# Kernel optimization log

Hardware: AMD Instinct MI355X
Metric: run time of the kernel (lower is better)

The kernel has to match this reference:

```python
import jax, jax.numpy as jnp
import numpy as np

B, T, E, H = 4, 1024, 1024, 16
D = E // H  # head_dim = 64


def setup_inputs() -> dict:
    key = jax.random.key(0)
    ks = jax.random.split(key, 6)
    s = 0.02  # realistic init scale for stable softmax
    return {
        "hidden_states": jax.random.normal(ks[0], (B, T, E), jnp.float32),
        "attention_mask": jnp.zeros((B, 1, T, T), jnp.float32),
        "Wq": jax.random.normal(ks[1], (E, E), jnp.float32) * s,
        "bq": jnp.zeros((E,), jnp.float32),
        "Wk": jax.random.normal(ks[2], (E, E), jnp.float32) * s,
        "bk": jnp.zeros((E,), jnp.float32),
        "Wv": jax.random.normal(ks[3], (E, E), jnp.float32) * s,
        "bv": jnp.zeros((E,), jnp.float32),
        "Wo": jax.random.normal(ks[4], (E, E), jnp.float32) * s,
        "bo": jnp.zeros((E,), jnp.float32),
    }


def reference(hidden_states, attention_mask, Wq, bq, Wk, bk, Wv, bv, Wo, bo):
    b, t, e = hidden_states.shape
    scaling = jnp.asarray(D, hidden_states.dtype) ** -0.5
    # q_proj weights/bias are pre-scaled in the module; equivalent to scaling q output
    q = (hidden_states @ Wq.T + bq) * scaling      # [B,T,E]
    k = hidden_states @ Wk.T + bk                   # self-attention path (no cache)
    v = hidden_states @ Wv.T + bv
    q = q.reshape(b, t, H, D)
    k = k.reshape(b, t, H, D)
    v = v.reshape(b, t, H, D)
    # bmm(q, k^T): [B,H,T,S] score matrix (materialized, as in the original)
    scores = jnp.einsum("bthd,bshd->bhts", q, k) + attention_mask
    probs = jax.nn.softmax(scores, axis=-1)
    ctx = jnp.einsum("bhts,bshd->bthd", probs, v).reshape(b, t, e)
    return ctx @ Wo.T + bo
```

## Files before the change

### kernel.cpp

```cpp
#include <hip/hip_runtime.h>
#include <math.h>

#define BB 4
#define TT 1024
#define EE 1024
#define HH 16
#define DD 64
#define KDIM 1024
#define N_HS (4096 * 1024)
#define N_W  (1024 * 1024)
#define NQKV (BB * HH * TT * DD)

typedef _Float16 f16x8 __attribute__((ext_vector_type(8)));
typedef float    f32x4 __attribute__((ext_vector_type(4)));

__device__ __forceinline__ unsigned short f2h(float x) {
    _Float16 h = (_Float16)x;
    return __builtin_bit_cast(unsigned short, h);
}
__device__ __forceinline__ void split_h(float x, unsigned short& hi, unsigned short& lo) {
    _Float16 h = (_Float16)x;
    hi = __builtin_bit_cast(unsigned short, h);
    lo = f2h(x - (float)h);
}

__device__ __forceinline__ void gload16(const void* g, void* l) {
    __builtin_amdgcn_global_load_lds(
        (const __attribute__((address_space(1))) void*)g,
        (__attribute__((address_space(3))) void*)l, 16, 0, 0);
}

__global__ __launch_bounds__(256)
void split_kernel(const float* __restrict__ hs,
                  const float* __restrict__ Wq, const float* __restrict__ Wk,
                  const float* __restrict__ Wv, const float* __restrict__ Wo,
                  unsigned short* __restrict__ ws)
{
    const int u = blockIdx.x * 256 + threadIdx.x;
    const float* src;
    unsigned short* dst;
    if (u < (N_HS / 4)) {
        src = hs + (size_t)u * 4;
        dst = ws + (size_t)u * 4;
    } else {
        int v = u - N_HS / 4;
        int wsel = v >> 18;
        int wo   = v & 0x3FFFF;
        const float* Wsrc = (wsel == 0) ? Wq : (wsel == 1) ? Wk : (wsel == 2) ? Wv : Wo;
        src = Wsrc + (size_t)wo * 4;
        dst = ws + (size_t)N_HS + (size_t)wsel * N_W + (size_t)wo * 4;
    }
    float4 x = *(const float4*)src;
    ushort4 h4;
    h4.x = f2h(x.x); h4.y = f2h(x.y); h4.z = f2h(x.z); h4.w = f2h(x.w);
    *(ushort4*)dst = h4;
}

__global__ __launch_bounds__(256)
void qkv_kernel(const unsigned short* __restrict__ hsp,
                const unsigned short* __restrict__ wqp,
                const float* __restrict__ bq, const float* __restrict__ bk,
                const float* __restrict__ bv,
                unsigned short* __restrict__ qkvb)
{
    __shared__ unsigned short Ah[128 * 32], Bh[128 * 32];

    const int widx  = blockIdx.x >> 3;
    const int nbase = (blockIdx.x & 7) * 128;
    const int mbase = blockIdx.y * 128;
    const unsigned short* Wp = wqp + (size_t)widx * N_W;
    const float* bias = (widx == 0) ? bq : (widx == 1) ? bk : bv;
    unsigned short* dst = qkvb + (size_t)widx * NQKV;
    const float scale = (widx == 0) ? 0.125f : 1.0f;

    const int tid  = threadIdx.x;
    const int w    = tid >> 6;
    const int lane = tid & 63;
    const int quad = lane >> 4;
    const int l16  = lane & 15;
    const int wm   = (w >> 1) * 64;
    const int wn   = (w & 1) * 64;

    f32x4 acc[4][4];
#pragma unroll
    for (int i = 0; i < 4; i++)
#pragma unroll
        for (int j = 0; j < 4; j++) acc[i][j] = (f32x4)0.f;

#pragma unroll 1
    for (int kt = 0; kt < KDIM; kt += 32) {
        __syncthreads();
#pragma unroll
        for (int i = 0; i < 2; i++) {
            int u = tid + i * 256;
            int r = u >> 2, c = u & 3;
            int q = c ^ ((r >> 1) & 3);
            gload16(hsp + (size_t)(mbase + r) * KDIM + kt + q * 8, &Ah[u * 8]);
            gload16(Wp  + (size_t)(nbase + r) * KDIM + kt + q * 8, &Bh[u * 8]);
        }
        __syncthreads();

        f16x8 af[4], bfr[4];
#pragma unroll
        for (int i = 0; i < 4; i++) {
            int r = wm + i * 16 + l16;
            af[i] = *(const f16x8*)&Ah[(r * 4 + (quad ^ ((r >> 1) & 3))) * 8];
        }
#pragma unroll
        for (int j = 0; j < 4; j++) {
            int r = wn + j * 16 + l16;
            bfr[j] = *(const f16x8*)&Bh[(r * 4 + (quad ^ ((r >> 1) & 3))) * 8];
        }
#pragma unroll
        for (int i = 0; i < 4; i++)
#pragma unroll
            for (int j = 0; j < 4; j++)
                acc[i][j] = __builtin_amdgcn_mfma_f32_16x16x32_f16(af[i], bfr[j], acc[i][j], 0, 0, 0);
    }

#pragma unroll
    for (int j = 0; j < 4; j++) {
        int n = nbase + wn + j * 16 + l16;
        int h = n >> 6, d = n & 63;
        float bj = bias[n];
#pragma unroll
        for (int i = 0; i < 4; i++)
#pragma unroll
            for (int rr = 0; rr < 4; rr++) {
                int m = mbase + wm + i * 16 + quad * 4 + rr;
                int b = m >> 10, t = m & 1023;
                dst[(((size_t)(b * HH + h) * TT + t) * DD + d)] =
                    f2h((acc[i][j][rr] + bj) * scale);
            }
    }
}

__global__ __launch_bounds__(256)
void vtrans_kernel(const unsigned short* __restrict__ vp,
                   unsigned short* __restrict__ vtp)
{
    __shared__ unsigned short Ts[64 * 72];
    const int bh = blockIdx.y;
    const int t0 = blockIdx.x * 64;
    const unsigned short* src = vp  + (size_t)bh * TT * DD + (size_t)t0 * DD;
    unsigned short*       dst = vtp + (size_t)bh * DD * TT + t0;
    const int tid = threadIdx.x;

#pragma unroll
    for (int i = 0; i < 2; i++) {
        int id = tid + i * 256;
        int r = id >> 3, c = id & 7;
        *(uint4*)&Ts[r * 72 + c * 8] = *(const uint4*)(src + (size_t)r * DD + c * 8);
    }
    __syncthreads();
#pragma unroll
    for (int i = 0; i < 2; i++) {
        int id = tid + i * 256;
        int d = id >> 3, c = id & 7;
        unsigned short tmp[8];
#pragma unroll
        for (int j = 0; j < 8; j++) tmp[j] = Ts[(c * 8 + j) * 72 + d];
        uint4 o;
        o.x = (unsigned int)tmp[0] | ((unsigned int)tmp[1] << 16);
        o.y = (unsigned int)tmp[2] | ((unsigned int)tmp[3] << 16);
        o.z = (unsigned int)tmp[4] | ((unsigned int)tmp[5] << 16);
        o.w = (unsigned int)tmp[6] | ((unsigned int)tmp[7] << 16);
        *(uint4*)(dst + (size_t)d * TT + c * 8) = o;
    }
}

__global__ __launch_bounds__(256)
void outproj_kernel(const unsigned short* __restrict__ ctxh,
                    const unsigned short* __restrict__ ctxl,
                    const unsigned short* __restrict__ wop,
                    const float* __restrict__ bo, float* __restrict__ out)
{
    __shared__ unsigned short Ach[64 * 32], Acl[64 * 32], Bh[128 * 32];

    const int nbase = blockIdx.x * 128;
    const int mbase = blockIdx.y * 64;

    const int tid  = threadIdx.x;
    const int w    = tid >> 6;
    const int lane = tid & 63;
    const int quad = lane >> 4;
    const int l16  = lane & 15;
    const int wm   = (w >> 1) * 32;
    const int wn   = (w & 1) * 64;

    f32x4 acc[2][4];
#pragma unroll
    for (int i = 0; i < 2; i++)
#pragma unroll
        for (int j = 0; j < 4; j++) acc[i][j] = (f32x4)0.f;

#pragma unroll 1
    for (int kt = 0; kt < KDIM; kt += 32) {
        __syncthreads();
        {
            int r = tid >> 2, c = tid & 3;
            int q = c ^ ((r >> 1) & 3);
            size_t ga = (size_t)(mbase + r) * KDIM + kt + q * 8;
            gload16(ctxh + ga, &Ach[tid * 8]);
            gload16(ctxl + ga, &Acl[tid * 8]);
        }
#pragma unroll
        for (int i = 0; i < 2; i++) {
            int u = tid + i * 256;
            int r = u >> 2, c = u & 3;
            int q = c ^ ((r >> 1) & 3);
            gload16(wop + (size_t)(nbase + r) * KDIM + kt + q * 8, &Bh[u * 8]);
        }
        __syncthreads();

        f16x8 ah[2], al[2], bfr[4];
#pragma unroll
        for (int i = 0; i < 2; i++) {
            int r = wm + i * 16 + l16;
            int slot = (r * 4 + (quad ^ ((r >> 1) & 3))) * 8;
            ah[i] = *(const f16x8*)&Ach[slot];
            al[i] = *(const f16x8*)&Acl[slot];
        }
#pragma unroll
        for (int j = 0; j < 4; j++) {
            int r = wn + j * 16 + l16;
            bfr[j] = *(const f16x8*)&Bh[(r * 4 + (quad ^ ((r >> 1) & 3))) * 8];
        }
#pragma unroll
        for (int i = 0; i < 2; i++)
#pragma unroll
            for (int j = 0; j < 4; j++) {
                acc[i][j] = __builtin_amdgcn_mfma_f32_16x16x32_f16(ah[i], bfr[j], acc[i][j], 0, 0, 0);
                acc[i][j] = __builtin_amdgcn_mfma_f32_16x16x32_f16(al[i], bfr[j], acc[i][j], 0, 0, 0);
            }
    }

#pragma unroll
    for (int j = 0; j < 4; j++) {
        int n = nbase + wn + j * 16 + l16;
        float bj = bo[n];
#pragma unroll
        for (int i = 0; i < 2; i++)
#pragma unroll
            for (int rr = 0; rr < 4; rr++) {
                int m = mbase + wm + i * 16 + quad * 4 + rr;
                out[(size_t)m * EE + n] = acc[i][j][rr] + bj;
            }
    }
}

#define LS 72

__global__ __launch_bounds__(256)
void attn_kernel(const unsigned short* __restrict__ qp_, const unsigned short* __restrict__ kp_,
                 const unsigned short* __restrict__ vtp_,
                 const float* __restrict__ mask,
                 unsigned short* __restrict__ ctxh, unsigned short* __restrict__ ctxl)
{
    __shared__ unsigned short Ks[64 * 64];
    __shared__ unsigned short Vt[64 * 64];
    __shared__ unsigned short Ps[64 * LS];

    const int bh = blockIdx.y;
    const int b  = bh >> 4;
    const int h  = bh & 15;
    const int m0 = blockIdx.x * 64;
    const size_t hoff = (size_t)bh * TT * DD;
    const unsigned short* qhp = qp_ + hoff;
    const unsigned short* khp = kp_ + hoff;
    const unsigned short* vtp = vtp_ + hoff;
    const float* mb = mask + (size_t)b * TT * TT;

    const int tid  = threadIdx.x;
    const int w    = tid >> 6;
    const int lane = tid & 63;
    const int quad = lane >> 4;
    const int l16  = lane & 15;

    f16x8 qf[2];
#pragma unroll
    for (int s = 0; s < 2; s++)
        qf[s] = *(const f16x8*)(qhp + (size_t)(m0 + w * 16 + l16) * DD + s * 32 + quad * 8);

    f32x4 o[4];
    float m_i[4], l_i[4];
#pragma unroll
    for (int t = 0; t < 4; t++) o[t] = (f32x4)0.f;
#pragma unroll
    for (int r = 0; r < 4; r++) { m_i[r] = -INFINITY; l_i[r] = 0.f; }

    for (int n0 = 0; n0 < TT; n0 += 64) {
        f32x4 st[4];
#pragma unroll
        for (int t = 0; t < 4; t++)
#pragma unroll
            for (int r = 0; r < 4; r++)
                st[t][r] = mb[(size_t)(m0 + w * 16 + quad * 4 + r) * TT + n0 + 16 * t + l16];

        __syncthreads();
#pragma unroll
        for (int i = 0; i < 2; i++) {
            int u = tid + i * 256;
            int r = u >> 3, cp = u & 7;
            int c = cp ^ (r & 7);
            gload16(khp + (size_t)(n0 + r) * DD + c * 8, &Ks[u * 8]);
            gload16(vtp + (size_t)r * TT + n0 + c * 8,   &Vt[u * 8]);
        }
        __syncthreads();

#pragma unroll
        for (int s = 0; s < 2; s++)
#pragma unroll
            for (int t = 0; t < 4; t++) {
                int R = 16 * t + l16;
                const f16x8 kf = *(const f16x8*)&Ks[(R * 8 + ((s * 4 + quad) ^ (R & 7))) * 8];
                st[t] = __builtin_amdgcn_mfma_f32_16x16x32_f16(qf[s], kf, st[t], 0, 0, 0);
            }

        float rm[4], rs[4], alpha[4];
#pragma unroll
        for (int r = 0; r < 4; r++)
            rm[r] = fmaxf(fmaxf(st[0][r], st[1][r]), fmaxf(st[2][r], st[3][r]));
#pragma unroll
        for (int mky = 1; mky < 16; mky <<= 1)
#pragma unroll
            for (int r = 0; r < 4; r++)
                rm[r] = fmaxf(rm[r], __shfl_xor(rm[r], mky));
#pragma unroll
        for (int r = 0; r < 4; r++) {
            float mn = fmaxf(m_i[r], rm[r]);
            alpha[r] = __expf(m_i[r] - mn);
            m_i[r]   = mn;
            rs[r]    = 0.f;
        }
#pragma unroll
        for (int t = 0; t < 4; t++)
#pragma unroll
            for (int r = 0; r < 4; r++) {
                float p = __expf(st[t][r] - m_i[r]);
                st[t][r] = p;
                rs[r] += p;
            }
#pragma unroll
        for (int mky = 1; mky < 16; mky <<= 1)
#pragma unroll
            for (int r = 0; r < 4; r++)
                rs[r] += __shfl_xor(rs[r], mky);
#pragma unroll
        for (int r = 0; r < 4; r++)
            l_i[r] = l_i[r] * alpha[r] + rs[r];
#pragma unroll
        for (int t = 0; t < 4; t++)
#pragma unroll
            for (int r = 0; r < 4; r++)
                o[t][r] *= alpha[r];

#pragma unroll
        for (int t = 0; t < 4; t++)
#pragma unroll
            for (int r = 0; r < 4; r++)
                Ps[(w * 16 + quad * 4 + r) * LS + 16 * t + l16] = f2h(st[t][r]);

#pragma unroll
        for (int s = 0; s < 2; s++) {
            const f16x8 pf = *(const f16x8*)&Ps[(w * 16 + l16) * LS + s * 32 + quad * 8];
#pragma unroll
            for (int t = 0; t < 4; t++) {
                int R = 16 * t + l16;
                const f16x8 vf = *(const f16x8*)&Vt[(R * 8 + ((s * 4 + quad) ^ (R & 7))) * 8];
                o[t] = __builtin_amdgcn_mfma_f32_16x16x32_f16(pf, vf, o[t], 0, 0, 0);
            }
        }
    }

#pragma unroll
    for (int r = 0; r < 4; r++) {
        float inv = 1.0f / l_i[r];
        int m = m0 + w * 16 + quad * 4 + r;
#pragma unroll
        for (int t = 0; t < 4; t++) {
            float val = o[t][r] * inv;
            unsigned short hi, lo;
            split_h(val, hi, lo);
            size_t off = (size_t)(b * TT + m) * EE + h * DD + 16 * t + l16;
            ctxh[off] = hi;
            ctxl[off] = lo;
        }
    }
}

extern "C" void kernel_launch(void* const* d_in, const int* in_sizes, int n_in,
                              void* d_out, int out_size, void* d_ws, size_t ws_size,
                              hipStream_t stream)
{
    const float* hs   = (const float*)d_in[0];
    const float* mask = (const float*)d_in[1];
    const float* Wq   = (const float*)d_in[2];
    const float* bq   = (const float*)d_in[3];
    const float* Wk   = (const float*)d_in[4];
    const float* bk   = (const float*)d_in[5];
    const float* Wv   = (const float*)d_in[6];
    const float* bv   = (const float*)d_in[7];
    const float* Wo   = (const float*)d_in[8];
    const float* bo   = (const float*)d_in[9];
    float* out = (float*)d_out;

    unsigned short* ws   = (unsigned short*)d_ws;
    unsigned short* hsp  = ws;
    unsigned short* wqp  = ws + (size_t)N_HS;
    unsigned short* wop  = wqp + 3 * (size_t)N_W;
    unsigned short* qkvb = wqp + 4 * (size_t)N_W;
    unsigned short* qp   = qkvb;
    unsigned short* kp   = qp + (size_t)NQKV;
    unsigned short* vp   = kp + (size_t)NQKV;
    unsigned short* ctxh = ws;
    unsigned short* ctxl = qkvb + 3 * (size_t)NQKV;
    unsigned short* vtp  = ctxl + (size_t)N_HS;

    split_kernel<<<8192, 256, 0, stream>>>(hs, Wq, Wk, Wv, Wo, ws);
    qkv_kernel<<<dim3(24, 32), 256, 0, stream>>>(hsp, wqp, bq, bk, bv, qkvb);
    vtrans_kernel<<<dim3(TT / 64, BB * HH), 256, 0, stream>>>(vp, vtp);
    attn_kernel<<<dim3(TT / 64, BB * HH), 256, 0, stream>>>(qp, kp, vtp, mask, ctxh, ctxl);
    outproj_kernel<<<dim3(8, 64), 256, 0, stream>>>(ctxh, ctxl, wop, bo, out);
}
```

Before: 232.4 us.

## Restructure attention as transposed S^T with double-buffered K/V and exp2 softmax

The attention kernel now computes transposed scores (K·Q^T) so each lane owns one query row, which removes most cross-lane shuffles. Probabilities stay in registers and feed a 16x16x16 MFMA directly instead of round-tripping through an LDS P tile. K/V tiles are double-buffered so the next tile loads while the current one computes, and exp2 with log2e folded into the Q scale and mask replaces exp. To make this work, a new kernel transposes and prescales the mask into workspace, which adds an extra 16 MB read and write pass and needs more workspace.

```diff
diff --git a/kernel.cpp b/kernel.cpp
--- a/kernel.cpp
+++ b/kernel.cpp
@@ -10,8 +10,10 @@
 #define N_HS (4096 * 1024)
 #define N_W  (1024 * 1024)
 #define NQKV (BB * HH * TT * DD)
+#define LOG2E 1.44269504088896340736f
 
 typedef _Float16 f16x8 __attribute__((ext_vector_type(8)));
+typedef _Float16 f16x4 __attribute__((ext_vector_type(4)));
 typedef float    f32x4 __attribute__((ext_vector_type(4)));
 
 __device__ __forceinline__ unsigned short f2h(float x) {
@@ -57,6 +59,38 @@
 }
 
 __global__ __launch_bounds__(256)
+void mtrans_kernel(const float* __restrict__ mask, float* __restrict__ mt)
+{
+    __shared__ float Ts[64][65];
+    const int b  = blockIdx.y;
+    const int m0 = (blockIdx.x & 15) * 64;
+    const int n0 = (blockIdx.x >> 4) * 64;
+    const float* src = mask + ((size_t)b * TT + m0) * TT + n0;
+    float*       dst = mt   + ((size_t)b * TT + n0) * TT + m0;
+    const int tid = threadIdx.x;
+#pragma unroll
+    for (int i = 0; i < 4; i++) {
+        int id = tid + i * 256;
+        int r = id >> 4, c = id & 15;
+        float4 v = *(const float4*)(src + (size_t)r * TT + c * 4);
+        Ts[r][c * 4 + 0] = v.x; Ts[r][c * 4 + 1] = v.y;
+        Ts[r][c * 4 + 2] = v.z; Ts[r][c * 4 + 3] = v.w;
+    }
+    __syncthreads();
+#pragma unroll
+    for (int i = 0; i < 4; i++) {
+        int id = tid + i * 256;
+        int d = id >> 4, c = id & 15;
+        float4 o;
+        o.x = Ts[c * 4 + 0][d] * LOG2E;
+        o.y = Ts[c * 4 + 1][d] * LOG2E;
+        o.z = Ts[c * 4 + 2][d] * LOG2E;
+        o.w = Ts[c * 4 + 3][d] * LOG2E;
+        *(float4*)(dst + (size_t)d * TT + c * 4) = o;
+    }
+}
+
+__global__ __launch_bounds__(256)
 void qkv_kernel(const unsigned short* __restrict__ hsp,
                 const unsigned short* __restrict__ wqp,
                 const float* __restrict__ bq, const float* __restrict__ bk,
@@ -71,7 +105,7 @@
     const unsigned short* Wp = wqp + (size_t)widx * N_W;
     const float* bias = (widx == 0) ? bq : (widx == 1) ? bk : bv;
     unsigned short* dst = qkvb + (size_t)widx * NQKV;
-    const float scale = (widx == 0) ? 0.125f : 1.0f;
+    const float scale = (widx == 0) ? 0.125f * LOG2E : 1.0f;
 
     const int tid  = threadIdx.x;
     const int w    = tid >> 6;
@@ -249,17 +283,14 @@
     }
 }
 
-#define LS 72
-
 __global__ __launch_bounds__(256)
 void attn_kernel(const unsigned short* __restrict__ qp_, const unsigned short* __restrict__ kp_,
                  const unsigned short* __restrict__ vtp_,
-                 const float* __restrict__ mask,
+                 const float* __restrict__ mtp,
                  unsigned short* __restrict__ ctxh, unsigned short* __restrict__ ctxl)
 {
-    __shared__ unsigned short Ks[64 * 64];
-    __shared__ unsigned short Vt[64 * 64];
-    __shared__ unsigned short Ps[64 * LS];
+    __shared__ unsigned short Ks[2][64 * 64];
+    __shared__ unsigned short Vt[2][64 * 64];
 
     const int bh = blockIdx.y;
     const int b  = bh >> 4;
@@ -269,124 +300,133 @@
     const unsigned short* qhp = qp_ + hoff;
     const unsigned short* khp = kp_ + hoff;
     const unsigned short* vtp = vtp_ + hoff;
-    const float* mb = mask + (size_t)b * TT * TT;
+    const float* mb = mtp + (size_t)b * TT * TT;
 
     const int tid  = threadIdx.x;
     const int w    = tid >> 6;
     const int lane = tid & 63;
     const int quad = lane >> 4;
     const int l16  = lane & 15;
+    const int m    = m0 + w * 16 + l16;
 
     f16x8 qf[2];
 #pragma unroll
     for (int s = 0; s < 2; s++)
-        qf[s] = *(const f16x8*)(qhp + (size_t)(m0 + w * 16 + l16) * DD + s * 32 + quad * 8);
-
-    f32x4 o[4];
-    float m_i[4], l_i[4];
-#pragma unroll
-    for (int t = 0; t < 4; t++) o[t] = (f32x4)0.f;
-#pragma unroll
-    for (int r = 0; r < 4; r++) { m_i[r] = -INFINITY; l_i[r] = 0.f; }
-
-    for (int n0 = 0; n0 < TT; n0 += 64) {
+        qf[s] = *(const f16x8*)(qhp + (size_t)m * DD + s * 32 + quad * 8);
+
+    f32x4 o2[4];
+#pragma unroll
+    for (int u = 0; u < 4; u++) o2[u] = (f32x4)0.f;
+    float m_i = -INFINITY, l_i = 0.f;
+
+#pragma unroll
+    for (int i = 0; i < 2; i++) {
+        int u = tid + i * 256;
+        int r = u >> 3, cp = u & 7;
+        int c = cp ^ (r & 7);
+        gload16(khp + (size_t)r * DD + c * 8, &Ks[0][u * 8]);
+        gload16(vtp + (size_t)r * TT + c * 8, &Vt[0][u * 8]);
+    }
+    __syncthreads();
+
+#pragma unroll 2
+    for (int it = 0; it < 16; ++it) {
+        const int n0  = it * 64;
+        const int cur = it & 1;
+
         f32x4 st[4];
 #pragma unroll
         for (int t = 0; t < 4; t++)
 #pragma unroll
             for (int r = 0; r < 4; r++)
-                st[t][r] = mb[(size_t)(m0 + w * 16 + quad * 4 + r) * TT + n0 + 16 * t + l16];
-
-        __syncthreads();
-#pragma unroll
-        for (int i = 0; i < 2; i++) {
-            int u = tid + i * 256;
-            int r = u >> 3, cp = u & 7;
-            int c = cp ^ (r & 7);
-            gload16(khp + (size_t)(n0 + r) * DD + c * 8, &Ks[u * 8]);
-            gload16(vtp + (size_t)r * TT + n0 + c * 8,   &Vt[u * 8]);
-        }
-        __syncthreads();
-
+                st[t][r] = mb[(size_t)(n0 + 16 * t + quad * 4 + r) * TT + m];
+
+        if (it < 15) {
+#pragma unroll
+            for (int i = 0; i < 2; i++) {
+                int u = tid + i * 256;
+                int r = u >> 3, cp = u & 7;
+                int c = cp ^ (r & 7);
+                gload16(khp + (size_t)(n0 + 64 + r) * DD + c * 8, &Ks[cur ^ 1][u * 8]);
+                gload16(vtp + (size_t)r * TT + n0 + 64 + c * 8,   &Vt[cur ^ 1][u * 8]);
+            }
+        }
+
+        __builtin_amdgcn_s_setprio(1);
 #pragma unroll
         for (int s = 0; s < 2; s++)
 #pragma unroll
             for (int t = 0; t < 4; t++) {
                 int R = 16 * t + l16;
-                const f16x8 kf = *(const f16x8*)&Ks[(R * 8 + ((s * 4 + quad) ^ (R & 7))) * 8];
-                st[t] = __builtin_amdgcn_mfma_f32_16x16x32_f16(qf[s], kf, st[t], 0, 0, 0);
-            }
-
-        float rm[4], rs[4], alpha[4];
-#pragma unroll
-        for (int r = 0; r < 4; r++)
-            rm[r] = fmaxf(fmaxf(st[0][r], st[1][r]), fmaxf(st[2][r], st[3][r]));
-#pragma unroll
-        for (int mky = 1; mky < 16; mky <<= 1)
-#pragma unroll
-            for (int r = 0; r < 4; r++)
-                rm[r] = fmaxf(rm[r], __shfl_xor(rm[r], mky));
-#pragma unroll
-        for (int r = 0; r < 4; r++) {
-            float mn = fmaxf(m_i[r], rm[r]);
-            alpha[r] = __expf(m_i[r] - mn);
-            m_i[r]   = mn;
-            rs[r]    = 0.f;
-        }
+                const f16x8 kf = *(const f16x8*)&Ks[cur][(R * 8 + ((s * 4 + quad) ^ (R & 7))) * 8];
+                st[t] = __builtin_amdgcn_mfma_f32_16x16x32_f16(kf, qf[s], st[t], 0, 0, 0);
+            }
+        __builtin_amdgcn_s_setprio(0);
+
+        float rm0 = fmaxf(fmaxf(st[0][0], st[0][1]), fmaxf(st[0][2], st[0][3]));
+        float rm1 = fmaxf(fmaxf(st[1][0], st[1][1]), fmaxf(st[1][2], st[1][3]));
+        float rm2 = fmaxf(fmaxf(st[2][0], st[2][1]), fmaxf(st[2][2], st[2][3]));
+        float rm3 = fmaxf(fmaxf(st[3][0], st[3][1]), fmaxf(st[3][2], st[3][3]));
+        float rm  = fmaxf(fmaxf(rm0, rm1), fmaxf(rm2, rm3));
+        rm = fmaxf(rm, __shfl_xor(rm, 16));
+        rm = fmaxf(rm, __shfl_xor(rm, 32));
+        float mn    = fmaxf(m_i, rm);
+        float alpha = exp2f(m_i - mn);
+        m_i = mn;
+        float rs = 0.f;
 #pragma unroll
         for (int t = 0; t < 4; t++)
 #pragma unroll
             for (int r = 0; r < 4; r++) {
-                float p = __expf(st[t][r] - m_i[r]);
+                float p = exp2f(st[t][r] - mn);
                 st[t][r] = p;
-                rs[r] += p;
-            }
-#pragma unroll
-        for (int mky = 1; mky < 16; mky <<= 1)
-#pragma unroll
-            for (int r = 0; r < 4; r++)
-                rs[r] += __shfl_xor(rs[r], mky);
-#pragma unroll
-        for (int r = 0; r < 4; r++)
-            l_i[r] = l_i[r] * alpha[r] + rs[r];
-#pragma unroll
-        for (int t = 0; t < 4; t++)
-#pragma unroll
-            for (int r = 0; r < 4; r++)
-                o[t][r] *= alpha[r];
-
-#pragma unroll
-        for (int t = 0; t < 4; t++)
-#pragma unroll
-            for (int r = 0; r < 4; r++)
-                Ps[(w * 16 + quad * 4 + r) * LS + 16 * t + l16] = f2h(st[t][r]);
-
-#pragma unroll
-        for (int s = 0; s < 2; s++) {
-            const f16x8 pf = *(const f16x8*)&Ps[(w * 16 + l16) * LS + s * 32 + quad * 8];
+                rs += p;
+            }
+        rs += __shfl_xor(rs, 16);
+        rs += __shfl_xor(rs, 32);
+        l_i = l_i * alpha + rs;
+
+        f16x4 pb[4];
+#pragma unroll
+        for (int t = 0; t < 4; t++) {
+            f16x4 pv;
+            pv[0] = (_Float16)st[t][0]; pv[1] = (_Float16)st[t][1];
+            pv[2] = (_Float16)st[t][2]; pv[3] = (_Float16)st[t][3];
+            pb[t] = pv;
+        }
+
+#pragma unroll
+        for (int u = 0; u < 4; u++)
+#pragma unroll
+            for (int rr = 0; rr < 4; rr++) o2[u][rr] *= alpha;
+
+        __builtin_amdgcn_s_setprio(1);
+#pragma unroll
+        for (int u = 0; u < 4; u++) {
+            int R = 16 * u + l16;
 #pragma unroll
             for (int t = 0; t < 4; t++) {
-                int R = 16 * t + l16;
-                const f16x8 vf = *(const f16x8*)&Vt[(R * 8 + ((s * 4 + quad) ^ (R & 7))) * 8];
-                o[t] = __builtin_amdgcn_mfma_f32_16x16x32_f16(pf, vf, o[t], 0, 0, 0);
-            }
-        }
-    }
-
-#pragma unroll
-    for (int r = 0; r < 4; r++) {
-        float inv = 1.0f / l_i[r];
-        int m = m0 + w * 16 + quad * 4 + r;
-#pragma unroll
-        for (int t = 0; t < 4; t++) {
-            float val = o[t][r] * inv;
+                const f16x4 vv = *(const f16x4*)&Vt[cur][(R * 8 + ((2 * t + (quad >> 1)) ^ (R & 7))) * 8 + (quad & 1) * 4];
+                o2[u] = __builtin_amdgcn_mfma_f32_16x16x16f16(vv, pb[t], o2[u], 0, 0, 0);
+            }
+        }
+        __builtin_amdgcn_s_setprio(0);
+
+        __syncthreads();
+    }
+
+    float inv = 1.0f / l_i;
+#pragma unroll
+    for (int u = 0; u < 4; u++)
+#pragma unroll
+        for (int rr = 0; rr < 4; rr++) {
+            float val = o2[u][rr] * inv;
             unsigned short hi, lo;
             split_h(val, hi, lo);
-            size_t off = (size_t)(b * TT + m) * EE + h * DD + 16 * t + l16;
+            size_t off = ((size_t)(b * TT + m)) * EE + h * DD + u * 16 + quad * 4 + rr;
             ctxh[off] = hi;
             ctxl[off] = lo;
         }
-    }
 }
 
 extern "C" void kernel_launch(void* const* d_in, const int* in_sizes, int n_in,
@@ -416,10 +456,12 @@
     unsigned short* ctxh = ws;
     unsigned short* ctxl = qkvb + 3 * (size_t)NQKV;
     unsigned short* vtp  = ctxl + (size_t)N_HS;
+    float*          mtp  = (float*)(vtp + (size_t)NQKV);
 
     split_kernel<<<8192, 256, 0, stream>>>(hs, Wq, Wk, Wv, Wo, ws);
+    mtrans_kernel<<<dim3(256, BB), 256, 0, stream>>>(mask, mtp);
     qkv_kernel<<<dim3(24, 32), 256, 0, stream>>>(hsp, wqp, bq, bk, bv, qkvb);
     vtrans_kernel<<<dim3(TT / 64, BB * HH), 256, 0, stream>>>(vp, vtp);
-    attn_kernel<<<dim3(TT / 64, BB * HH), 256, 0, stream>>>(qp, kp, vtp, mask, ctxh, ctxl);
+    attn_kernel<<<dim3(TT / 64, BB * HH), 256, 0, stream>>>(qp, kp, vtp, mtp, ctxh, ctxl);
     outproj_kernel<<<dim3(8, 64), 256, 0, stream>>>(ctxh, ctxl, wop, bo, out);
 }
```

After: 233.6 us. About the same (+0.6%).
